# Performance work log

Measured on AMD Instinct MI355X. Metric: run time of the kernel, lower is better.

The kernel has to match this reference:

```python
import jax, jax.numpy as jnp
import numpy as np

N, E = 50000, 800000
IN_CH, INTER, H1, H2 = 256, 32, 8, 8
C2 = IN_CH // H2  # 32
NEG_SLOPE = 0.2


def setup_inputs() -> dict:
    key = jax.random.key(0)
    ks = jax.random.split(key, 10)
    x = jax.random.normal(ks[0], (N, IN_CH), dtype=jnp.float32)
    edge_index = jax.random.randint(ks[1], (2, E), 0, N, dtype=jnp.int32)
    s = 0.05
    W1 = jax.random.normal(ks[2], (H1 * INTER, IN_CH), dtype=jnp.float32) * s
    att_src1 = jax.random.normal(ks[3], (1, H1, INTER), dtype=jnp.float32) * s
    att_dst1 = jax.random.normal(ks[4], (1, H1, INTER), dtype=jnp.float32) * s
    b1 = jnp.zeros((H1 * INTER,), dtype=jnp.float32)
    W2 = jax.random.normal(ks[5], (H2 * C2, H1 * INTER), dtype=jnp.float32) * s
    att_src2 = jax.random.normal(ks[6], (1, H2, C2), dtype=jnp.float32) * s
    att_dst2 = jax.random.normal(ks[7], (1, H2, C2), dtype=jnp.float32) * s
    b2 = jnp.zeros((H2 * C2,), dtype=jnp.float32)
    return {"x": x, "edge_index": edge_index,
            "W1": W1, "att_src1": att_src1, "att_dst1": att_dst1, "b1": b1,
            "W2": W2, "att_src2": att_src2, "att_dst2": att_dst2, "b2": b2}


def gat_conv(x, edge_index, W, att_src, att_dst, bias, H, C):
    # PyG GATConv (shared lin for src/dst, add_self_loops=False, concat=True)
    n = x.shape[0]
    src, dst = edge_index[0], edge_index[1]
    xw = (x @ W.T).reshape(n, H, C)                     # [N,H,C]
    a_src = jnp.sum(xw * att_src, axis=-1)              # [N,H]
    a_dst = jnp.sum(xw * att_dst, axis=-1)              # [N,H]
    e = a_src[src] + a_dst[dst]                         # [E,H]
    e = jnp.where(e >= 0, e, NEG_SLOPE * e)             # LeakyReLU(0.2)
    # segment softmax over edges grouped by destination node
    m = jax.ops.segment_max(e, dst, num_segments=n)     # [N,H]
    ex = jnp.exp(e - m[dst])
    denom = jax.ops.segment_sum(ex, dst, num_segments=n)
    alpha = ex / (denom[dst] + 1e-16)                   # [E,H]
    # weighted scatter-aggregate of source messages
    msg = xw[src] * alpha[:, :, None]                   # [E,H,C]
    out = jax.ops.segment_sum(msg, dst, num_segments=n) # [N,H,C]
    return out.reshape(n, H * C) + bias


def reference(x, edge_index, W1, att_src1, att_dst1, b1, W2, att_src2, att_dst2, b2):
    h = gat_conv(x, edge_index, W1, att_src1, att_dst1, b1, H1, INTER)
    h = jax.nn.gelu(h, approximate=False)  # F.gelu default is exact
    h = gat_conv(h, edge_index, W2, att_src2, att_dst2, b2, H2, C2)
    return h[-1]  # eval-path super node
```

## Files before the change

kernel.cpp:

```cpp
#include <hip/hip_runtime.h>
#include <math.h>

#define N_NODES 50000
#define N_EDGES 800000
#define C2MAX 512
#define K1MAX 512
#define E1MAX 8192
#define N2MAX 2048
#define DEGMAX 1024

__global__ void k_find2(const int* __restrict__ esrc, const int* __restrict__ edst,
                        int* cnt, int* slot1, int* e2src) {
    int i = blockIdx.x * blockDim.x + threadIdx.x;
    if (i == 0) slot1[N_NODES - 1] = -2;
    if (i >= N_EDGES) return;
    if (edst[i] == N_NODES - 1) {
        int s = esrc[i];
        int j = atomicAdd(&cnt[0], 1);
        if (j < C2MAX) e2src[j] = s;
        slot1[s] = -2;
    }
}

__global__ void k_compact1(int* cnt, int* slot1, int* nodes1) {
    int u = blockIdx.x * blockDim.x + threadIdx.x;
    if (u >= N_NODES) return;
    if (slot1[u] == -2) {
        int k = atomicAdd(&cnt[1], 1);
        if (k < K1MAX) { slot1[u] = k; nodes1[k] = u; }
        else slot1[u] = -1;
    }
}

__global__ void k_find1(const int* __restrict__ esrc, const int* __restrict__ edst,
                        int* cnt, const int* __restrict__ slot1,
                        const int* __restrict__ nodes1,
                        int* l1k, int* l1src, int* slot2) {
    int i = blockIdx.x * blockDim.x + threadIdx.x;
    int K1 = min(cnt[1], K1MAX);
    if (i < K1) slot2[nodes1[i]] = -2;
    if (i >= N_EDGES) return;
    int d = edst[i];
    int k = slot1[d];
    if (k >= 0) {
        int s = esrc[i];
        int j = atomicAdd(&cnt[2], 1);
        if (j < E1MAX) { l1k[j] = k; l1src[j] = s; slot2[s] = -2; }
    }
}

__global__ void k_compact2(int* cnt, int* slot2, int* nodes2) {
    int u = blockIdx.x * blockDim.x + threadIdx.x;
    if (u >= N_NODES) return;
    if (slot2[u] == -2) {
        int m = atomicAdd(&cnt[3], 1);
        if (m < N2MAX) { slot2[u] = m; nodes2[m] = u; }
        else slot2[u] = -1;
    }
}

__global__ void k_xw1(const float* __restrict__ x, const float* __restrict__ W,
                      const float* __restrict__ attS, const float* __restrict__ attD,
                      const int* cnt, const int* __restrict__ nodes2,
                      float* xw1, float* as1, float* ad1) {
    int b = blockIdx.x;
    int n2 = min(cnt[3], N2MAX);
    if (b >= n2) return;
    int t = threadIdx.x;
    int u = nodes2[b];
    __shared__ float xs[256];
    __shared__ float redS[256], redD[256];
    xs[t] = x[(size_t)u * 256 + t];
    __syncthreads();
    const float* wrow = W + (size_t)t * 256;
    float acc = 0.f;
#pragma unroll 8
    for (int c = 0; c < 256; ++c) acc = fmaf(xs[c], wrow[c], acc);
    xw1[(size_t)b * 256 + t] = acc;
    redS[t] = acc * attS[t];
    redD[t] = acc * attD[t];
    __syncthreads();
    if ((t & 31) == 0) {
        int h = t >> 5;
        float s = 0.f, d = 0.f;
        for (int i = 0; i < 32; ++i) { s += redS[t + i]; d += redD[t + i]; }
        as1[b * 8 + h] = s;
        ad1[b * 8 + h] = d;
    }
}

__global__ void k_attn1(const int* cnt, const int* __restrict__ nodes1,
                        const int* __restrict__ slot2,
                        const int* __restrict__ l1k, const int* __restrict__ l1src,
                        const float* __restrict__ xw1, const float* __restrict__ as1,
                        const float* __restrict__ ad1,
                        const float* __restrict__ b1, float* h1g) {
    int k = blockIdx.x;
    int K1 = min(cnt[1], K1MAX);
    if (k >= K1) return;
    int t = threadIdx.x;
    int h = t >> 5;
    int c1 = min(cnt[2], E1MAX);
    __shared__ int elist[DEGMAX];
    __shared__ int ecnt;
    if (t == 0) ecnt = 0;
    __syncthreads();
    for (int j = t; j < c1; j += 256) {
        if (l1k[j] == k) {
            int p = atomicAdd(&ecnt, 1);
            if (p < DEGMAX) elist[p] = l1src[j];
        }
    }
    __syncthreads();
    int ne = min(ecnt, DEGMAX);
    int u = nodes1[k];
    float adst = ad1[slot2[u] * 8 + h];
    float m = -INFINITY;
    for (int j = 0; j < ne; ++j) {
        int s2 = slot2[elist[j]];
        float e = as1[s2 * 8 + h] + adst;
        e = (e >= 0.f) ? e : 0.2f * e;
        m = fmaxf(m, e);
    }
    float denom = 0.f, acc = 0.f;
    for (int j = 0; j < ne; ++j) {
        int s2 = slot2[elist[j]];
        float e = as1[s2 * 8 + h] + adst;
        e = (e >= 0.f) ? e : 0.2f * e;
        float p = expf(e - m);
        denom += p;
        acc = fmaf(p, xw1[(size_t)s2 * 256 + t], acc);
    }
    float out = (ne > 0) ? acc / (denom + 1e-16f) : 0.f;
    out += b1[t];
    float g = 0.5f * out * (1.f + erff(out * 0.70710678118654752440f));
    h1g[(size_t)k * 256 + t] = g;
}

__global__ void k_xw2(const float* __restrict__ h1g, const float* __restrict__ W,
                      const float* __restrict__ attS, const float* __restrict__ attD,
                      const int* cnt, float* xw2, float* as2, float* ad2) {
    int b = blockIdx.x;
    int K1 = min(cnt[1], K1MAX);
    if (b >= K1) return;
    int t = threadIdx.x;
    __shared__ float xs[256];
    __shared__ float redS[256], redD[256];
    xs[t] = h1g[(size_t)b * 256 + t];
    __syncthreads();
    const float* wrow = W + (size_t)t * 256;
    float acc = 0.f;
#pragma unroll 8
    for (int c = 0; c < 256; ++c) acc = fmaf(xs[c], wrow[c], acc);
    xw2[(size_t)b * 256 + t] = acc;
    redS[t] = acc * attS[t];
    redD[t] = acc * attD[t];
    __syncthreads();
    if ((t & 31) == 0) {
        int h = t >> 5;
        float s = 0.f, d = 0.f;
        for (int i = 0; i < 32; ++i) { s += redS[t + i]; d += redD[t + i]; }
        as2[b * 8 + h] = s;
        ad2[b * 8 + h] = d;
    }
}

__global__ void k_final(const int* cnt, const int* __restrict__ slot1,
                        const int* __restrict__ e2src,
                        const float* __restrict__ xw2, const float* __restrict__ as2,
                        const float* __restrict__ ad2,
                        const float* __restrict__ b2, float* __restrict__ out) {
    int t = threadIdx.x;
    int h = t >> 5;
    int c2 = min(cnt[0], C2MAX);
    int kd = slot1[N_NODES - 1];
    __shared__ int eslot[C2MAX];
    for (int j = t; j < c2; j += 256) eslot[j] = slot1[e2src[j]];
    __syncthreads();
    float adst = ad2[kd * 8 + h];
    float m = -INFINITY;
    for (int j = 0; j < c2; ++j) {
        float e = as2[eslot[j] * 8 + h] + adst;
        e = (e >= 0.f) ? e : 0.2f * e;
        m = fmaxf(m, e);
    }
    float denom = 0.f, acc = 0.f;
    for (int j = 0; j < c2; ++j) {
        int kk = eslot[j];
        float e = as2[kk * 8 + h] + adst;
        e = (e >= 0.f) ? e : 0.2f * e;
        float p = expf(e - m);
        denom += p;
        acc = fmaf(p, xw2[(size_t)kk * 256 + t], acc);
    }
    float o = (c2 > 0) ? acc / (denom + 1e-16f) : 0.f;
    out[t] = o + b2[t];
}

extern "C" void kernel_launch(void* const* d_in, const int* in_sizes, int n_in,
                              void* d_out, int out_size, void* d_ws, size_t ws_size,
                              hipStream_t stream) {
    const float* x    = (const float*)d_in[0];
    const int*   eidx = (const int*)d_in[1];
    const int*   esrc = eidx;
    const int*   edst = eidx + N_EDGES;
    const float* W1   = (const float*)d_in[2];
    const float* aS1  = (const float*)d_in[3];
    const float* aD1  = (const float*)d_in[4];
    const float* b1   = (const float*)d_in[5];
    const float* W2   = (const float*)d_in[6];
    const float* aS2  = (const float*)d_in[7];
    const float* aD2  = (const float*)d_in[8];
    const float* b2   = (const float*)d_in[9];
    float* out = (float*)d_out;

    char* p = (char*)d_ws;
    int* cnt    = (int*)p; p += 256;
    int* slot1  = (int*)p; p += N_NODES * sizeof(int);
    int* slot2  = (int*)p; p += N_NODES * sizeof(int);
    int* e2src  = (int*)p; p += C2MAX * sizeof(int);
    int* l1k    = (int*)p; p += E1MAX * sizeof(int);
    int* l1src  = (int*)p; p += E1MAX * sizeof(int);
    int* nodes1 = (int*)p; p += K1MAX * sizeof(int);
    int* nodes2 = (int*)p; p += N2MAX * sizeof(int);
    float* xw1  = (float*)p; p += (size_t)N2MAX * 256 * sizeof(float);
    float* as1  = (float*)p; p += (size_t)N2MAX * 8 * sizeof(float);
    float* ad1  = (float*)p; p += (size_t)N2MAX * 8 * sizeof(float);
    float* h1g  = (float*)p; p += (size_t)K1MAX * 256 * sizeof(float);
    float* xw2  = (float*)p; p += (size_t)K1MAX * 256 * sizeof(float);
    float* as2  = (float*)p; p += (size_t)K1MAX * 8 * sizeof(float);
    float* ad2  = (float*)p; p += (size_t)K1MAX * 8 * sizeof(float);

    hipMemsetAsync(cnt, 0, 256, stream);
    hipMemsetAsync(slot1, 0xFF, 2 * N_NODES * sizeof(int), stream);

    const int EB = (N_EDGES + 255) / 256;
    const int NB = (N_NODES + 255) / 256;

    k_find2  <<<EB, 256, 0, stream>>>(esrc, edst, cnt, slot1, e2src);
    k_compact1<<<NB, 256, 0, stream>>>(cnt, slot1, nodes1);
    k_find1  <<<EB, 256, 0, stream>>>(esrc, edst, cnt, slot1, nodes1, l1k, l1src, slot2);
    k_compact2<<<NB, 256, 0, stream>>>(cnt, slot2, nodes2);
    k_xw1    <<<N2MAX, 256, 0, stream>>>(x, W1, aS1, aD1, cnt, nodes2, xw1, as1, ad1);
    k_attn1  <<<K1MAX, 256, 0, stream>>>(cnt, nodes1, slot2, l1k, l1src, xw1, as1, ad1, b1, h1g);
    k_xw2    <<<K1MAX, 256, 0, stream>>>(h1g, W2, aS2, aD2, cnt, xw2, as2, ad2);
    k_final  <<<1, 256, 0, stream>>>(cnt, slot1, e2src, xw2, as2, ad2, b2, out);
}
```

Before: 150.8 us.

## Fuse all GAT stages into one cooperative persistent kernel with grid syncs

Replaces eight separate kernel launches and two memsets with a single cooperative kernel of 512 blocks that runs every stage and separates them with grid-wide barriers. Workspace initialisation moves inside the kernel, and the edge scans and weight row reads use 128-bit vector loads. The aim is to remove per-launch overhead and memset dispatch cost. In exchange it adds eight grid.sync barriers, and the edge scans now run on far fewer threads than the original one-thread-per-edge launches.

```diff
diff --git a/kernel.cpp b/kernel.cpp
--- a/kernel.cpp
+++ b/kernel.cpp
@@ -1,5 +1,8 @@
 #include <hip/hip_runtime.h>
+#include <hip/hip_cooperative_groups.h>
 #include <math.h>
+
+namespace cg = cooperative_groups;
 
 #define N_NODES 50000
 #define N_EDGES 800000
@@ -9,192 +12,233 @@
 #define N2MAX 2048
 #define DEGMAX 1024
 
-__global__ void k_find2(const int* __restrict__ esrc, const int* __restrict__ edst,
-                        int* cnt, int* slot1, int* e2src) {
-    int i = blockIdx.x * blockDim.x + threadIdx.x;
-    if (i == 0) slot1[N_NODES - 1] = -2;
-    if (i >= N_EDGES) return;
-    if (edst[i] == N_NODES - 1) {
-        int s = esrc[i];
-        int j = atomicAdd(&cnt[0], 1);
-        if (j < C2MAX) e2src[j] = s;
-        slot1[s] = -2;
-    }
-}
-
-__global__ void k_compact1(int* cnt, int* slot1, int* nodes1) {
-    int u = blockIdx.x * blockDim.x + threadIdx.x;
-    if (u >= N_NODES) return;
-    if (slot1[u] == -2) {
-        int k = atomicAdd(&cnt[1], 1);
-        if (k < K1MAX) { slot1[u] = k; nodes1[k] = u; }
-        else slot1[u] = -1;
-    }
-}
-
-__global__ void k_find1(const int* __restrict__ esrc, const int* __restrict__ edst,
-                        int* cnt, const int* __restrict__ slot1,
-                        const int* __restrict__ nodes1,
-                        int* l1k, int* l1src, int* slot2) {
-    int i = blockIdx.x * blockDim.x + threadIdx.x;
-    int K1 = min(cnt[1], K1MAX);
-    if (i < K1) slot2[nodes1[i]] = -2;
-    if (i >= N_EDGES) return;
-    int d = edst[i];
-    int k = slot1[d];
-    if (k >= 0) {
-        int s = esrc[i];
-        int j = atomicAdd(&cnt[2], 1);
-        if (j < E1MAX) { l1k[j] = k; l1src[j] = s; slot2[s] = -2; }
-    }
-}
-
-__global__ void k_compact2(int* cnt, int* slot2, int* nodes2) {
-    int u = blockIdx.x * blockDim.x + threadIdx.x;
-    if (u >= N_NODES) return;
-    if (slot2[u] == -2) {
-        int m = atomicAdd(&cnt[3], 1);
-        if (m < N2MAX) { slot2[u] = m; nodes2[m] = u; }
-        else slot2[u] = -1;
-    }
-}
-
-__global__ void k_xw1(const float* __restrict__ x, const float* __restrict__ W,
-                      const float* __restrict__ attS, const float* __restrict__ attD,
-                      const int* cnt, const int* __restrict__ nodes2,
-                      float* xw1, float* as1, float* ad1) {
-    int b = blockIdx.x;
-    int n2 = min(cnt[3], N2MAX);
-    if (b >= n2) return;
-    int t = threadIdx.x;
-    int u = nodes2[b];
+#define GRID_BLKS 512
+
+__global__ void gat_fused(const float* __restrict__ x,
+                          const int* __restrict__ eidx,
+                          const float* __restrict__ W1, const float* __restrict__ aS1,
+                          const float* __restrict__ aD1, const float* __restrict__ b1,
+                          const float* __restrict__ W2, const float* __restrict__ aS2,
+                          const float* __restrict__ aD2, const float* __restrict__ b2,
+                          float* __restrict__ out, char* __restrict__ ws) {
+    cg::grid_group grid = cg::this_grid();
+    const int t = threadIdx.x;
+    const int tid = blockIdx.x * blockDim.x + t;
+    const int nthreads = gridDim.x * blockDim.x;
+
+    const int* esrc = eidx;
+    const int* edst = eidx + N_EDGES;
+
+    int* cnt    = (int*)ws;
+    int* slot1  = (int*)(ws + 256);
+    int* slot2  = slot1 + N_NODES;
+    int* e2src  = slot2 + N_NODES;
+    int* l1k    = e2src + C2MAX;
+    int* l1src  = l1k + E1MAX;
+    int* nodes1 = l1src + E1MAX;
+    int* nodes2 = nodes1 + K1MAX;
+    float* xw1  = (float*)(nodes2 + N2MAX);
+    float* as1  = xw1 + (size_t)N2MAX * 256;
+    float* ad1  = as1 + N2MAX * 8;
+    float* h1g  = ad1 + N2MAX * 8;
+    float* xw2  = h1g + (size_t)K1MAX * 256;
+    float* as2  = xw2 + (size_t)K1MAX * 256;
+    float* ad2  = as2 + K1MAX * 8;
+
     __shared__ float xs[256];
     __shared__ float redS[256], redD[256];
-    xs[t] = x[(size_t)u * 256 + t];
-    __syncthreads();
-    const float* wrow = W + (size_t)t * 256;
-    float acc = 0.f;
-#pragma unroll 8
-    for (int c = 0; c < 256; ++c) acc = fmaf(xs[c], wrow[c], acc);
-    xw1[(size_t)b * 256 + t] = acc;
-    redS[t] = acc * attS[t];
-    redD[t] = acc * attD[t];
-    __syncthreads();
-    if ((t & 31) == 0) {
+    __shared__ int   s_elist[DEGMAX];
+    __shared__ int   s_ecnt;
+    __shared__ int   s_eslot[C2MAX];
+
+    for (int u = tid; u < N_NODES; u += nthreads) { slot1[u] = -1; slot2[u] = -1; }
+    if (tid < 8) cnt[tid] = 0;
+    grid.sync();
+
+    if (tid == 0) slot1[N_NODES - 1] = -2;
+    {
+        const int4* edst4 = (const int4*)edst;
+        for (int i = tid; i < N_EDGES / 4; i += nthreads) {
+            int4 d = edst4[i];
+            #pragma unroll
+            for (int j = 0; j < 4; ++j) {
+                int dj = (j == 0) ? d.x : (j == 1) ? d.y : (j == 2) ? d.z : d.w;
+                if (dj == N_NODES - 1) {
+                    int s = esrc[4 * i + j];
+                    int p = atomicAdd(&cnt[0], 1);
+                    if (p < C2MAX) e2src[p] = s;
+                    slot1[s] = -2;
+                }
+            }
+        }
+    }
+    grid.sync();
+
+    for (int u = tid; u < N_NODES; u += nthreads) {
+        if (slot1[u] == -2) {
+            int k = atomicAdd(&cnt[1], 1);
+            if (k < K1MAX) { slot1[u] = k; nodes1[k] = u; }
+            else slot1[u] = -1;
+        }
+    }
+    grid.sync();
+
+    {
+        int K1 = min(cnt[1], K1MAX);
+        for (int i = tid; i < K1; i += nthreads) slot2[nodes1[i]] = -2;
+        const int4* edst4 = (const int4*)edst;
+        for (int i = tid; i < N_EDGES / 4; i += nthreads) {
+            int4 d = edst4[i];
+            #pragma unroll
+            for (int j = 0; j < 4; ++j) {
+                int dj = (j == 0) ? d.x : (j == 1) ? d.y : (j == 2) ? d.z : d.w;
+                int k = slot1[dj];
+                if (k >= 0) {
+                    int s = esrc[4 * i + j];
+                    int p = atomicAdd(&cnt[2], 1);
+                    if (p < E1MAX) { l1k[p] = k; l1src[p] = s; slot2[s] = -2; }
+                }
+            }
+        }
+    }
+    grid.sync();
+
+    for (int u = tid; u < N_NODES; u += nthreads) {
+        if (slot2[u] == -2) {
+            int m = atomicAdd(&cnt[3], 1);
+            if (m < N2MAX) { slot2[u] = m; nodes2[m] = u; }
+            else slot2[u] = -1;
+        }
+    }
+    grid.sync();
+
+    {
+        int n2 = min(cnt[3], N2MAX);
+        for (int b = blockIdx.x; b < n2; b += gridDim.x) {
+            int u = nodes2[b];
+            xs[t] = x[(size_t)u * 256 + t];
+            __syncthreads();
+            const float4* wrow = (const float4*)(W1 + (size_t)t * 256);
+            float acc = 0.f;
+            #pragma unroll 8
+            for (int c = 0; c < 64; ++c) {
+                float4 w = wrow[c];
+                float4 xv = *(const float4*)&xs[4 * c];
+                acc = fmaf(xv.x, w.x, acc); acc = fmaf(xv.y, w.y, acc);
+                acc = fmaf(xv.z, w.z, acc); acc = fmaf(xv.w, w.w, acc);
+            }
+            xw1[(size_t)b * 256 + t] = acc;
+            redS[t] = acc * aS1[t];
+            redD[t] = acc * aD1[t];
+            __syncthreads();
+            if ((t & 31) == 0) {
+                int h = t >> 5;
+                float s = 0.f, d = 0.f;
+                for (int i = 0; i < 32; ++i) { s += redS[t + i]; d += redD[t + i]; }
+                as1[b * 8 + h] = s;
+                ad1[b * 8 + h] = d;
+            }
+            __syncthreads();
+        }
+    }
+    grid.sync();
+
+    {
+        int K1 = min(cnt[1], K1MAX);
+        int c1 = min(cnt[2], E1MAX);
         int h = t >> 5;
-        float s = 0.f, d = 0.f;
-        for (int i = 0; i < 32; ++i) { s += redS[t + i]; d += redD[t + i]; }
-        as1[b * 8 + h] = s;
-        ad1[b * 8 + h] = d;
-    }
-}
-
-__global__ void k_attn1(const int* cnt, const int* __restrict__ nodes1,
-                        const int* __restrict__ slot2,
-                        const int* __restrict__ l1k, const int* __restrict__ l1src,
-                        const float* __restrict__ xw1, const float* __restrict__ as1,
-                        const float* __restrict__ ad1,
-                        const float* __restrict__ b1, float* h1g) {
-    int k = blockIdx.x;
-    int K1 = min(cnt[1], K1MAX);
-    if (k >= K1) return;
-    int t = threadIdx.x;
-    int h = t >> 5;
-    int c1 = min(cnt[2], E1MAX);
-    __shared__ int elist[DEGMAX];
-    __shared__ int ecnt;
-    if (t == 0) ecnt = 0;
-    __syncthreads();
-    for (int j = t; j < c1; j += 256) {
-        if (l1k[j] == k) {
-            int p = atomicAdd(&ecnt, 1);
-            if (p < DEGMAX) elist[p] = l1src[j];
-        }
-    }
-    __syncthreads();
-    int ne = min(ecnt, DEGMAX);
-    int u = nodes1[k];
-    float adst = ad1[slot2[u] * 8 + h];
-    float m = -INFINITY;
-    for (int j = 0; j < ne; ++j) {
-        int s2 = slot2[elist[j]];
-        float e = as1[s2 * 8 + h] + adst;
-        e = (e >= 0.f) ? e : 0.2f * e;
-        m = fmaxf(m, e);
-    }
-    float denom = 0.f, acc = 0.f;
-    for (int j = 0; j < ne; ++j) {
-        int s2 = slot2[elist[j]];
-        float e = as1[s2 * 8 + h] + adst;
-        e = (e >= 0.f) ? e : 0.2f * e;
-        float p = expf(e - m);
-        denom += p;
-        acc = fmaf(p, xw1[(size_t)s2 * 256 + t], acc);
-    }
-    float out = (ne > 0) ? acc / (denom + 1e-16f) : 0.f;
-    out += b1[t];
-    float g = 0.5f * out * (1.f + erff(out * 0.70710678118654752440f));
-    h1g[(size_t)k * 256 + t] = g;
-}
-
-__global__ void k_xw2(const float* __restrict__ h1g, const float* __restrict__ W,
-                      const float* __restrict__ attS, const float* __restrict__ attD,
-                      const int* cnt, float* xw2, float* as2, float* ad2) {
-    int b = blockIdx.x;
-    int K1 = min(cnt[1], K1MAX);
-    if (b >= K1) return;
-    int t = threadIdx.x;
-    __shared__ float xs[256];
-    __shared__ float redS[256], redD[256];
-    xs[t] = h1g[(size_t)b * 256 + t];
-    __syncthreads();
-    const float* wrow = W + (size_t)t * 256;
-    float acc = 0.f;
-#pragma unroll 8
-    for (int c = 0; c < 256; ++c) acc = fmaf(xs[c], wrow[c], acc);
-    xw2[(size_t)b * 256 + t] = acc;
-    redS[t] = acc * attS[t];
-    redD[t] = acc * attD[t];
-    __syncthreads();
-    if ((t & 31) == 0) {
+        for (int k = blockIdx.x; k < K1; k += gridDim.x) {
+            if (t == 0) s_ecnt = 0;
+            __syncthreads();
+            for (int j = t; j < c1; j += 256) {
+                if (l1k[j] == k) {
+                    int p = atomicAdd(&s_ecnt, 1);
+                    if (p < DEGMAX) s_elist[p] = l1src[j];
+                }
+            }
+            __syncthreads();
+            int ne = min(s_ecnt, DEGMAX);
+            int u = nodes1[k];
+            float adst = ad1[slot2[u] * 8 + h];
+            float m = -INFINITY;
+            for (int j = 0; j < ne; ++j) {
+                int s2 = slot2[s_elist[j]];
+                float e = as1[s2 * 8 + h] + adst;
+                e = (e >= 0.f) ? e : 0.2f * e;
+                m = fmaxf(m, e);
+            }
+            float denom = 0.f, acc = 0.f;
+            for (int j = 0; j < ne; ++j) {
+                int s2 = slot2[s_elist[j]];
+                float e = as1[s2 * 8 + h] + adst;
+                e = (e >= 0.f) ? e : 0.2f * e;
+                float p = expf(e - m);
+                denom += p;
+                acc = fmaf(p, xw1[(size_t)s2 * 256 + t], acc);
+            }
+            float o = (ne > 0) ? acc / (denom + 1e-16f) : 0.f;
+            o += b1[t];
+            h1g[(size_t)k * 256 + t] = 0.5f * o * (1.f + erff(o * 0.70710678118654752440f));
+            __syncthreads();
+        }
+    }
+    grid.sync();
+
+    {
+        int K1 = min(cnt[1], K1MAX);
+        for (int b = blockIdx.x; b < K1; b += gridDim.x) {
+            xs[t] = h1g[(size_t)b * 256 + t];
+            __syncthreads();
+            const float4* wrow = (const float4*)(W2 + (size_t)t * 256);
+            float acc = 0.f;
+            #pragma unroll 8
+            for (int c = 0; c < 64; ++c) {
+                float4 w = wrow[c];
+                float4 xv = *(const float4*)&xs[4 * c];
+                acc = fmaf(xv.x, w.x, acc); acc = fmaf(xv.y, w.y, acc);
+                acc = fmaf(xv.z, w.z, acc); acc = fmaf(xv.w, w.w, acc);
+            }
+            xw2[(size_t)b * 256 + t] = acc;
+            redS[t] = acc * aS2[t];
+            redD[t] = acc * aD2[t];
+            __syncthreads();
+            if ((t & 31) == 0) {
+                int h = t >> 5;
+                float s = 0.f, d = 0.f;
+                for (int i = 0; i < 32; ++i) { s += redS[t + i]; d += redD[t + i]; }
+                as2[b * 8 + h] = s;
+                ad2[b * 8 + h] = d;
+            }
+            __syncthreads();
+        }
+    }
+    grid.sync();
+
+    if (blockIdx.x == 0) {
         int h = t >> 5;
-        float s = 0.f, d = 0.f;
-        for (int i = 0; i < 32; ++i) { s += redS[t + i]; d += redD[t + i]; }
-        as2[b * 8 + h] = s;
-        ad2[b * 8 + h] = d;
-    }
-}
-
-__global__ void k_final(const int* cnt, const int* __restrict__ slot1,
-                        const int* __restrict__ e2src,
-                        const float* __restrict__ xw2, const float* __restrict__ as2,
-                        const float* __restrict__ ad2,
-                        const float* __restrict__ b2, float* __restrict__ out) {
-    int t = threadIdx.x;
-    int h = t >> 5;
-    int c2 = min(cnt[0], C2MAX);
-    int kd = slot1[N_NODES - 1];
-    __shared__ int eslot[C2MAX];
-    for (int j = t; j < c2; j += 256) eslot[j] = slot1[e2src[j]];
-    __syncthreads();
-    float adst = ad2[kd * 8 + h];
-    float m = -INFINITY;
-    for (int j = 0; j < c2; ++j) {
-        float e = as2[eslot[j] * 8 + h] + adst;
-        e = (e >= 0.f) ? e : 0.2f * e;
-        m = fmaxf(m, e);
-    }
-    float denom = 0.f, acc = 0.f;
-    for (int j = 0; j < c2; ++j) {
-        int kk = eslot[j];
-        float e = as2[kk * 8 + h] + adst;
-        e = (e >= 0.f) ? e : 0.2f * e;
-        float p = expf(e - m);
-        denom += p;
-        acc = fmaf(p, xw2[(size_t)kk * 256 + t], acc);
-    }
-    float o = (c2 > 0) ? acc / (denom + 1e-16f) : 0.f;
-    out[t] = o + b2[t];
+        int c2 = min(cnt[0], C2MAX);
+        int kd = slot1[N_NODES - 1];
+        for (int j = t; j < c2; j += 256) s_eslot[j] = slot1[e2src[j]];
+        __syncthreads();
+        float adst = ad2[kd * 8 + h];
+        float m = -INFINITY;
+        for (int j = 0; j < c2; ++j) {
+            float e = as2[s_eslot[j] * 8 + h] + adst;
+            e = (e >= 0.f) ? e : 0.2f * e;
+            m = fmaxf(m, e);
+        }
+        float denom = 0.f, acc = 0.f;
+        for (int j = 0; j < c2; ++j) {
+            int kk = s_eslot[j];
+            float e = as2[kk * 8 + h] + adst;
+            e = (e >= 0.f) ? e : 0.2f * e;
+            float p = expf(e - m);
+            denom += p;
+            acc = fmaf(p, xw2[(size_t)kk * 256 + t], acc);
+        }
+        float o = (c2 > 0) ? acc / (denom + 1e-16f) : 0.f;
+        out[t] = o + b2[t];
+    }
 }
 
 extern "C" void kernel_launch(void* const* d_in, const int* in_sizes, int n_in,
@@ -202,8 +246,6 @@
                               hipStream_t stream) {
     const float* x    = (const float*)d_in[0];
     const int*   eidx = (const int*)d_in[1];
-    const int*   esrc = eidx;
-    const int*   edst = eidx + N_EDGES;
     const float* W1   = (const float*)d_in[2];
     const float* aS1  = (const float*)d_in[3];
     const float* aD1  = (const float*)d_in[4];
@@ -213,36 +255,12 @@
     const float* aD2  = (const float*)d_in[8];
     const float* b2   = (const float*)d_in[9];
     float* out = (float*)d_out;
-
-    char* p = (char*)d_ws;
-    int* cnt    = (int*)p; p += 256;
-    int* slot1  = (int*)p; p += N_NODES * sizeof(int);
-    int* slot2  = (int*)p; p += N_NODES * sizeof(int);
-    int* e2src  = (int*)p; p += C2MAX * sizeof(int);
-    int* l1k    = (int*)p; p += E1MAX * sizeof(int);
-    int* l1src  = (int*)p; p += E1MAX * sizeof(int);
-    int* nodes1 = (int*)p; p += K1MAX * sizeof(int);
-    int* nodes2 = (int*)p; p += N2MAX * sizeof(int);
-    float* xw1  = (float*)p; p += (size_t)N2MAX * 256 * sizeof(float);
-    float* as1  = (float*)p; p += (size_t)N2MAX * 8 * sizeof(float);
-    float* ad1  = (float*)p; p += (size_t)N2MAX * 8 * sizeof(float);
-    float* h1g  = (float*)p; p += (size_t)K1MAX * 256 * sizeof(float);
-    float* xw2  = (float*)p; p += (size_t)K1MAX * 256 * sizeof(float);
-    float* as2  = (float*)p; p += (size_t)K1MAX * 8 * sizeof(float);
-    float* ad2  = (float*)p; p += (size_t)K1MAX * 8 * sizeof(float);
-
-    hipMemsetAsync(cnt, 0, 256, stream);
-    hipMemsetAsync(slot1, 0xFF, 2 * N_NODES * sizeof(int), stream);
-
-    const int EB = (N_EDGES + 255) / 256;
-    const int NB = (N_NODES + 255) / 256;
-
-    k_find2  <<<EB, 256, 0, stream>>>(esrc, edst, cnt, slot1, e2src);
-    k_compact1<<<NB, 256, 0, stream>>>(cnt, slot1, nodes1);
-    k_find1  <<<EB, 256, 0, stream>>>(esrc, edst, cnt, slot1, nodes1, l1k, l1src, slot2);
-    k_compact2<<<NB, 256, 0, stream>>>(cnt, slot2, nodes2);
-    k_xw1    <<<N2MAX, 256, 0, stream>>>(x, W1, aS1, aD1, cnt, nodes2, xw1, as1, ad1);
-    k_attn1  <<<K1MAX, 256, 0, stream>>>(cnt, nodes1, slot2, l1k, l1src, xw1, as1, ad1, b1, h1g);
-    k_xw2    <<<K1MAX, 256, 0, stream>>>(h1g, W2, aS2, aD2, cnt, xw2, as2, ad2);
-    k_final  <<<1, 256, 0, stream>>>(cnt, slot1, e2src, xw2, as2, ad2, b2, out);
+    char*  ws  = (char*)d_ws;
+
+    void* args[] = {
+        (void*)&x, (void*)&eidx, (void*)&W1, (void*)&aS1, (void*)&aD1, (void*)&b1,
+        (void*)&W2, (void*)&aS2, (void*)&aD2, (void*)&b2, (void*)&out, (void*)&ws
+    };
+    hipLaunchCooperativeKernel((const void*)gat_fused, dim3(GRID_BLKS), dim3(256),
+                               args, 0, stream);
 }
```

Measured after the change: 576.0 us. 3.82x slower.
